# Optimization experiments

Measured on AMD Instinct MI355X. Metric: run time of the kernel, lower is better.

The kernel has to match this reference:

```python
import jax, jax.numpy as jnp
import numpy as np

B, IN_DIM, HID = 4096, 1024, 1024


def setup_inputs() -> dict:
    key = jax.random.key(0)
    ks = jax.random.split(key, 6)
    x_t = jax.random.normal(ks[0], (B, IN_DIM), dtype=jnp.float32)
    h_prev = jax.random.normal(ks[1], (B, HID), dtype=jnp.float32)
    c_prev = jax.random.normal(ks[2], (B, HID), dtype=jnp.float32)
    # stacked input-proj weights for gates (f, i, o, g): [4H, in_dim]
    U_w = jax.random.normal(ks[3], (4 * HID, IN_DIM), dtype=jnp.float32) * (1.0 / np.sqrt(IN_DIM))
    # biases: zeros except forget-gate bias = 1.0 (matches Uf.bias.fill_(1.0))
    U_b = jnp.concatenate([jnp.ones((HID,), jnp.float32), jnp.zeros((3 * HID,), jnp.float32)])
    # stacked hidden-proj weights (no bias): [4H, H]
    W_w = jax.random.normal(ks[4], (4 * HID, HID), dtype=jnp.float32) * (1.0 / np.sqrt(HID))
    return {"x_t": x_t, "h_prev": h_prev, "c_prev": c_prev,
            "U_w": U_w, "U_b": U_b, "W_w": W_w}


def reference(x_t, h_prev, c_prev, U_w, U_b, W_w):
    # two concatenated GEMMs covering all 8 original Linear layers
    pre = x_t @ U_w.T + U_b + h_prev @ W_w.T  # [B, 4H]
    f_pre, i_pre, o_pre, g_pre = jnp.split(pre, 4, axis=-1)
    f_t = jax.nn.sigmoid(f_pre)
    i_t = jax.nn.sigmoid(i_pre)
    o_t = jax.nn.sigmoid(o_pre)
    g_t = jnp.tanh(g_pre)
    c_t = f_t * c_prev + i_t * g_t
    h_t = o_t * jnp.tanh(c_t)
    return (h_t, c_t)
```

## Files before the change

### kernel.cpp

```cpp
#include <hip/hip_runtime.h>
#include <hip/hip_bf16.h>


#define BATCH 4096
#define HID   1024
#define KDIM  2048

#define BM 256
#define BN 256
#define BK 32
#define NT (KDIM / BK)
#define SLOT_E (BM * BK)

typedef __bf16 bf16x8 __attribute__((ext_vector_type(8)));
typedef float  f32x4  __attribute__((ext_vector_type(4)));

__device__ __forceinline__ void async_load16(const void* g, void* l) {
    __builtin_amdgcn_global_load_lds(
        (const __attribute__((address_space(1))) void*)g,
        (__attribute__((address_space(3))) void*)l,
        16, 0, 0);
}

__device__ __forceinline__ float sigmoidf_(float v) {
    return 1.0f / (1.0f + __expf(-v));
}
__device__ __forceinline__ float tanhf_(float v) {
    return 1.0f - 2.0f / (__expf(2.0f * v) + 1.0f);
}

__global__ __launch_bounds__(256) void convert_kernel(
    const float* __restrict__ x, const float* __restrict__ h,
    const float* __restrict__ U, const float* __restrict__ W,
    __hip_bfloat16* __restrict__ Acat, __hip_bfloat16* __restrict__ Bcat)
{
    const int CH_PER_MAT = (4096 * KDIM) / 8;
    int idx = blockIdx.x * blockDim.x + threadIdx.x;
    bool isB = idx >= CH_PER_MAT;
    int c = isB ? (idx - CH_PER_MAT) : idx;
    int row  = c >> 8;
    int col  = (c & 255) << 3;
    int srow = row;
    if (isB) {
        int g  = (row >> 4) & 3;
        int j  = ((row >> 8) << 6) + (((row >> 6) & 3) << 4) + (row & 15);
        srow = g * 1024 + j;
    }
    const float* src;
    if (col < 1024) src = (isB ? U : x) + (size_t)srow * 1024 + col;
    else            src = (isB ? W : h) + (size_t)srow * 1024 + (col - 1024);
    float4 v0 = *(const float4*)(src);
    float4 v1 = *(const float4*)(src + 4);
    __hip_bfloat16 tmp[8];
    tmp[0] = __float2bfloat16(v0.x); tmp[1] = __float2bfloat16(v0.y);
    tmp[2] = __float2bfloat16(v0.z); tmp[3] = __float2bfloat16(v0.w);
    tmp[4] = __float2bfloat16(v1.x); tmp[5] = __float2bfloat16(v1.y);
    tmp[6] = __float2bfloat16(v1.z); tmp[7] = __float2bfloat16(v1.w);
    __hip_bfloat16* dst = (isB ? Bcat : Acat) + (size_t)row * KDIM + col;
    *(bf16x8*)dst = *(const bf16x8*)tmp;
}

__global__ __launch_bounds__(512, 2) void gemm_lstm_kernel(
    const __hip_bfloat16* __restrict__ A,
    const __hip_bfloat16* __restrict__ Bm,
    const float* __restrict__ Ub,
    const float* __restrict__ c_prev,
    float* __restrict__ out)
{
    __shared__ __align__(16) __hip_bfloat16 smem[4 * 2 * SLOT_E];

    const int tid  = threadIdx.x;
    const int lane = tid & 63;
    const int wid  = tid >> 6;
    const int wm   = wid >> 2;
    const int wn   = wid & 3;

    int wg  = blockIdx.x;
    int wgs = (wg & 7) * (256 / 8) + (wg >> 3);
    const int bm = wgs >> 4;
    const int bn = wgs & 15;

    const __hip_bfloat16* Ab = A  + (size_t)bm * BM * KDIM;
    const __hip_bfloat16* Bb = Bm + (size_t)bn * BN * KDIM;

    const int frow = lane & 15;
    const int sp8  = (((lane >> 4) ^ ((frow >> 1) & 3)) << 3);
    const int arow = wm * 128 + frow;
    const int brow = wn * 64  + frow;

    const int c0 = tid,        c1 = 512 + tid;
    const int r0 = c0 >> 2,    r1 = c1 >> 2;
    const int g0 = ((c0 & 3) ^ ((r0 >> 1) & 3)) << 3;
    const int g1 = ((c1 & 3) ^ ((r1 >> 1) & 3)) << 3;
    const size_t ga0 = (size_t)r0 * KDIM + g0;
    const size_t ga1 = (size_t)r1 * KDIM + g1;
    const int l0 = c0 << 3,    l1 = c1 << 3;

    f32x4 acc[8][4] = {};

#define STAGE_A(kt, slot) do { \
    int _ko = (kt) * BK; unsigned _b = (unsigned)((slot) * 2 + 0) * SLOT_E; \
    async_load16(Ab + ga0 + _ko, &smem[_b + l0]); \
    async_load16(Ab + ga1 + _ko, &smem[_b + l1]); } while (0)
#define STAGE_B(kt, slot) do { \
    int _ko = (kt) * BK; unsigned _b = (unsigned)((slot) * 2 + 1) * SLOT_E; \
    async_load16(Bb + ga0 + _ko, &smem[_b + l0]); \
    async_load16(Bb + ga1 + _ko, &smem[_b + l1]); } while (0)

    STAGE_A(0, 0); STAGE_B(0, 0);
    STAGE_A(1, 1); STAGE_B(1, 1);
    STAGE_A(2, 2); STAGE_B(2, 2);
    asm volatile("s_waitcnt vmcnt(8)" ::: "memory");
    __builtin_amdgcn_s_barrier();

    for (int t = 0; t < NT; ++t) {
        const int slot = t & 3;
        const unsigned ab = (unsigned)(slot * 2 + 0) * SLOT_E;
        const unsigned bb = (unsigned)(slot * 2 + 1) * SLOT_E;
        int tp = t + 3; if (tp > NT - 1) tp = NT - 1;
        const int ps = (t + 3) & 3;

        STAGE_A(tp, ps);
        STAGE_B(tp, ps);

        bf16x8 ar[4], br[4];
#pragma unroll
        for (int m = 0; m < 4; ++m)
            ar[m] = *(const bf16x8*)&smem[ab + (unsigned)((arow + m * 16) * BK) + sp8];
#pragma unroll
        for (int n = 0; n < 4; ++n)
            br[n] = *(const bf16x8*)&smem[bb + (unsigned)((brow + n * 16) * BK) + sp8];

        __builtin_amdgcn_s_setprio(1);
#pragma unroll
        for (int m = 0; m < 4; ++m)
#pragma unroll
            for (int n = 0; n < 4; ++n)
                acc[m][n] = __builtin_amdgcn_mfma_f32_16x16x32_bf16(ar[m], br[n], acc[m][n], 0, 0, 0);
        __builtin_amdgcn_s_setprio(0);

        bf16x8 ar2[4];
#pragma unroll
        for (int m = 0; m < 4; ++m)
            ar2[m] = *(const bf16x8*)&smem[ab + (unsigned)((arow + 64 + m * 16) * BK) + sp8];

        __builtin_amdgcn_s_setprio(1);
#pragma unroll
        for (int m = 0; m < 4; ++m)
#pragma unroll
            for (int n = 0; n < 4; ++n)
                acc[m + 4][n] = __builtin_amdgcn_mfma_f32_16x16x32_bf16(ar2[m], br[n], acc[m + 4][n], 0, 0, 0);
        __builtin_amdgcn_s_setprio(0);

        asm volatile("s_waitcnt vmcnt(8)" ::: "memory");
        __builtin_amdgcn_s_barrier();
    }
#undef STAGE_A
#undef STAGE_B

    const int j = bn * 64 + wn * 16 + (lane & 15);
    const float bf_ = Ub[j];
    const float bi_ = Ub[1024 + j];
    const float bo_ = Ub[2048 + j];
    const float bg_ = Ub[3072 + j];
    const int row0 = bm * BM + wm * 128 + ((lane >> 4) << 2);

    float cp[8][4];
#pragma unroll
    for (int m = 0; m < 8; ++m)
#pragma unroll
        for (int r = 0; r < 4; ++r)
            cp[m][r] = c_prev[(size_t)(row0 + m * 16 + r) * HID + j];

#pragma unroll
    for (int m = 0; m < 8; ++m) {
#pragma unroll
        for (int r = 0; r < 4; ++r) {
            const int row = row0 + m * 16 + r;
            const float f  = sigmoidf_(acc[m][0][r] + bf_);
            const float it = sigmoidf_(acc[m][1][r] + bi_);
            const float o  = sigmoidf_(acc[m][2][r] + bo_);
            const float gg = tanhf_(acc[m][3][r] + bg_);
            const float cv = f * cp[m][r] + it * gg;
            const float hv = o * tanhf_(cv);
            out[(size_t)row * HID + j] = hv;
            out[(size_t)BATCH * HID + (size_t)row * HID + j] = cv;
        }
    }
}

extern "C" void kernel_launch(void* const* d_in, const int* in_sizes, int n_in,
                              void* d_out, int out_size, void* d_ws, size_t ws_size,
                              hipStream_t stream) {
    const float* x      = (const float*)d_in[0];
    const float* h_prev = (const float*)d_in[1];
    const float* c_prev = (const float*)d_in[2];
    const float* U_w    = (const float*)d_in[3];
    const float* U_b    = (const float*)d_in[4];
    const float* W_w    = (const float*)d_in[5];
    float* out = (float*)d_out;

    char* ws = (char*)d_ws;
    __hip_bfloat16* Acat = (__hip_bfloat16*)ws;
    __hip_bfloat16* Bcat = (__hip_bfloat16*)(ws + (16u << 20));

    convert_kernel<<<8192, 256, 0, stream>>>(x, h_prev, U_w, W_w, Acat, Bcat);
    gemm_lstm_kernel<<<256, 512, 0, stream>>>(Acat, Bcat, U_b, c_prev, out);
}
```

Baseline: 91.53 us.

## Restructure GEMM main loop into BK=64 ping-pong schedule with interleaved staging

Doubles the K tile to 64 and replaces the 4-slot ring buffer with two 64KB buffers. Each buffer holds A and B halves that are refilled per half-tile, interleaved between MFMA phases with explicit lgkm/vm waits and sched barriers. The even/odd register sets double-buffer the LDS fragment reads. The XCD-aware block mapping changes to group tiles into 4x8 regions, and launch bounds drop to one block per CU because of the 128KB LDS. The aim is better overlap of global loads, LDS reads and MFMAs and better L2 locality, at the cost of occupancy.

Result: faster. 83.62 us (-8.6%).

```diff
diff --git a/kernel.cpp b/kernel.cpp
--- a/kernel.cpp
+++ b/kernel.cpp
@@ -8,9 +8,8 @@
 
 #define BM 256
 #define BN 256
-#define BK 32
-#define NT (KDIM / BK)
-#define SLOT_E (BM * BK)
+#define BK 64
+#define NITER (KDIM / (2 * BK))
 
 typedef __bf16 bf16x8 __attribute__((ext_vector_type(8)));
 typedef float  f32x4  __attribute__((ext_vector_type(4)));
@@ -60,14 +59,14 @@
     *(bf16x8*)dst = *(const bf16x8*)tmp;
 }
 
-__global__ __launch_bounds__(512, 2) void gemm_lstm_kernel(
+__global__ __launch_bounds__(512, 1) void gemm_lstm_kernel(
     const __hip_bfloat16* __restrict__ A,
     const __hip_bfloat16* __restrict__ Bm,
     const float* __restrict__ Ub,
     const float* __restrict__ c_prev,
     float* __restrict__ out)
 {
-    __shared__ __align__(16) __hip_bfloat16 smem[4 * 2 * SLOT_E];
+    __shared__ __align__(16) unsigned char smem[131072];
 
     const int tid  = threadIdx.x;
     const int lane = tid & 63;
@@ -76,87 +75,124 @@
     const int wn   = wid & 3;
 
     int wg  = blockIdx.x;
-    int wgs = (wg & 7) * (256 / 8) + (wg >> 3);
-    const int bm = wgs >> 4;
-    const int bn = wgs & 15;
+    const int xcd = wg & 7;
+    const int i_  = wg >> 3;
+    const int bm = ((xcd >> 1) << 2) + (i_ >> 3);
+    const int bn = ((xcd & 1) << 3) + (i_ & 7);
 
     const __hip_bfloat16* Ab = A  + (size_t)bm * BM * KDIM;
     const __hip_bfloat16* Bb = Bm + (size_t)bn * BN * KDIM;
 
     const int frow = lane & 15;
-    const int sp8  = (((lane >> 4) ^ ((frow >> 1) & 3)) << 3);
-    const int arow = wm * 128 + frow;
-    const int brow = wn * 64  + frow;
-
-    const int c0 = tid,        c1 = 512 + tid;
-    const int r0 = c0 >> 2,    r1 = c1 >> 2;
-    const int g0 = ((c0 & 3) ^ ((r0 >> 1) & 3)) << 3;
-    const int g1 = ((c1 & 3) ^ ((r1 >> 1) & 3)) << 3;
-    const size_t ga0 = (size_t)r0 * KDIM + g0;
-    const size_t ga1 = (size_t)r1 * KDIM + g1;
-    const int l0 = c0 << 3,    l1 = c1 << 3;
+    const int kq   = lane >> 4;
+    const int esw  = (frow >> 1) & 7;
+    const unsigned xs0 = (unsigned)((kq ^ esw) << 4);
+    const unsigned xs1 = xs0 ^ 64u;
+    const unsigned wmBase = (unsigned)wm * 16384u;
+    const unsigned bnBase = (unsigned)(wn >> 1) * 16384u;
+    const unsigned bnRow  = (unsigned)(wn & 1) * 64u;
+
+    const int ch0 = tid,           ch1 = 512 + tid;
+    const int sr0 = ch0 >> 3,      sr1 = ch1 >> 3;
+    const int sc0 = ((ch0 & 7) ^ ((sr0 >> 1) & 7)) << 3;
+    const int sc1 = ((ch1 & 7) ^ ((sr1 >> 1) & 7)) << 3;
+    const size_t ga0 = (size_t)sr0 * KDIM + sc0;
+    const size_t ga1 = (size_t)sr1 * KDIM + sc1;
 
     f32x4 acc[8][4] = {};
-
-#define STAGE_A(kt, slot) do { \
-    int _ko = (kt) * BK; unsigned _b = (unsigned)((slot) * 2 + 0) * SLOT_E; \
-    async_load16(Ab + ga0 + _ko, &smem[_b + l0]); \
-    async_load16(Ab + ga1 + _ko, &smem[_b + l1]); } while (0)
-#define STAGE_B(kt, slot) do { \
-    int _ko = (kt) * BK; unsigned _b = (unsigned)((slot) * 2 + 1) * SLOT_E; \
-    async_load16(Bb + ga0 + _ko, &smem[_b + l0]); \
-    async_load16(Bb + ga1 + _ko, &smem[_b + l1]); } while (0)
-
-    STAGE_A(0, 0); STAGE_B(0, 0);
-    STAGE_A(1, 1); STAGE_B(1, 1);
-    STAGE_A(2, 2); STAGE_B(2, 2);
-    asm volatile("s_waitcnt vmcnt(8)" ::: "memory");
-    __builtin_amdgcn_s_barrier();
-
-    for (int t = 0; t < NT; ++t) {
-        const int slot = t & 3;
-        const unsigned ab = (unsigned)(slot * 2 + 0) * SLOT_E;
-        const unsigned bb = (unsigned)(slot * 2 + 1) * SLOT_E;
-        int tp = t + 3; if (tp > NT - 1) tp = NT - 1;
-        const int ps = (t + 3) & 3;
-
-        STAGE_A(tp, ps);
-        STAGE_B(tp, ps);
-
-        bf16x8 ar[4], br[4];
-#pragma unroll
-        for (int m = 0; m < 4; ++m)
-            ar[m] = *(const bf16x8*)&smem[ab + (unsigned)((arow + m * 16) * BK) + sp8];
-#pragma unroll
-        for (int n = 0; n < 4; ++n)
-            br[n] = *(const bf16x8*)&smem[bb + (unsigned)((brow + n * 16) * BK) + sp8];
-
-        __builtin_amdgcn_s_setprio(1);
-#pragma unroll
-        for (int m = 0; m < 4; ++m)
-#pragma unroll
-            for (int n = 0; n < 4; ++n)
-                acc[m][n] = __builtin_amdgcn_mfma_f32_16x16x32_bf16(ar[m], br[n], acc[m][n], 0, 0, 0);
-        __builtin_amdgcn_s_setprio(0);
-
-        bf16x8 ar2[4];
-#pragma unroll
-        for (int m = 0; m < 4; ++m)
-            ar2[m] = *(const bf16x8*)&smem[ab + (unsigned)((arow + 64 + m * 16) * BK) + sp8];
-
-        __builtin_amdgcn_s_setprio(1);
-#pragma unroll
-        for (int m = 0; m < 4; ++m)
-#pragma unroll
-            for (int n = 0; n < 4; ++n)
-                acc[m + 4][n] = __builtin_amdgcn_mfma_f32_16x16x32_bf16(ar2[m], br[n], acc[m + 4][n], 0, 0, 0);
-        __builtin_amdgcn_s_setprio(0);
-
-        asm volatile("s_waitcnt vmcnt(8)" ::: "memory");
-        __builtin_amdgcn_s_barrier();
+    bf16x8 arE[4], arO[4], brE[4], brO[4];
+
+#define RD16(B) (*(const bf16x8*)(smem + (B)))
+#define LDA4(SET, BUFB, MH, XS) do { \
+    const unsigned _b = (BUFB) + wmBase; \
+    SET[0] = RD16(_b + (unsigned)((MH)*64 +  0 + frow)*128u + (XS)); \
+    SET[1] = RD16(_b + (unsigned)((MH)*64 + 16 + frow)*128u + (XS)); \
+    SET[2] = RD16(_b + (unsigned)((MH)*64 + 32 + frow)*128u + (XS)); \
+    SET[3] = RD16(_b + (unsigned)((MH)*64 + 48 + frow)*128u + (XS)); } while (0)
+#define LDB4(SET, BUFB, XS) do { \
+    const unsigned _b = (BUFB) + 32768u + bnBase; \
+    SET[0] = RD16(_b + (bnRow +  0 + frow)*128u + (XS)); \
+    SET[1] = RD16(_b + (bnRow + 16 + frow)*128u + (XS)); \
+    SET[2] = RD16(_b + (bnRow + 32 + frow)*128u + (XS)); \
+    SET[3] = RD16(_b + (bnRow + 48 + frow)*128u + (XS)); } while (0)
+#define STG_A(TSRC, BUFB, H) do { \
+    const unsigned _rg = (BUFB) + (H)*16384u; \
+    const __hip_bfloat16* _s = Ab + (size_t)(H)*128*KDIM + (size_t)(TSRC)*64; \
+    async_load16(_s + ga0, smem + _rg + (unsigned)ch0*16u); \
+    async_load16(_s + ga1, smem + _rg + (unsigned)ch1*16u); } while (0)
+#define STG_B(TSRC, BUFB, H) do { \
+    const unsigned _rg = (BUFB) + 32768u + (H)*16384u; \
+    const __hip_bfloat16* _s = Bb + (size_t)(H)*128*KDIM + (size_t)(TSRC)*64; \
+    async_load16(_s + ga0, smem + _rg + (unsigned)ch0*16u); \
+    async_load16(_s + ga1, smem + _rg + (unsigned)ch1*16u); } while (0)
+#define MF16(ASET, BSET, MB) do { \
+    __builtin_amdgcn_s_setprio(1); \
+    _Pragma("unroll") for (int _m = 0; _m < 4; ++_m) \
+    _Pragma("unroll") for (int _n = 0; _n < 4; ++_n) \
+        acc[(MB)+_m][_n] = __builtin_amdgcn_mfma_f32_16x16x32_bf16( \
+            ASET[_m], BSET[_n], acc[(MB)+_m][_n], 0, 0, 0); \
+    __builtin_amdgcn_s_setprio(0); } while (0)
+#define DRAIN_LGKM asm volatile("s_waitcnt lgkmcnt(0)" ::: "memory")
+#define WAIT_VM4   asm volatile("s_waitcnt vmcnt(4)" ::: "memory")
+#define PH_BAR do { __builtin_amdgcn_sched_barrier(0); \
+                    __builtin_amdgcn_s_barrier(); } while (0)
+
+    STG_B(0, 0u, 0); STG_B(0, 0u, 1);
+    STG_A(0, 0u, 0); STG_A(0, 0u, 1);
+    STG_B(1, 65536u, 0); STG_B(1, 65536u, 1);
+    STG_A(1, 65536u, 0);
+    asm volatile("s_waitcnt vmcnt(6)" ::: "memory");
+    PH_BAR;
+    LDA4(arE, 0u, 0, xs0); LDB4(brE, 0u, xs0);
+
+#pragma unroll 1
+    for (int i = 0; i < NITER; ++i) {
+        const int tb = 2 * i + 1;
+        const int tc = (2 * i + 2 < 32) ? 2 * i + 2 : 31;
+        const int td = (2 * i + 3 < 32) ? 2 * i + 3 : 31;
+
+        LDA4(arO, 0u, 0, xs1); LDB4(brO, 0u, xs1);
+        STG_A(tb, 65536u, 1);
+        MF16(arE, brE, 0);
+        DRAIN_LGKM; PH_BAR;
+        LDA4(arE, 0u, 1, xs0);
+        STG_B(tc, 0u, 0);
+        MF16(arO, brO, 0);
+        PH_BAR;
+        LDA4(arO, 0u, 1, xs1);
+        STG_B(tc, 0u, 1);
+        MF16(arE, brE, 4);
+        DRAIN_LGKM; WAIT_VM4; PH_BAR;
+        LDA4(arE, 65536u, 0, xs0); LDB4(brE, 65536u, xs0);
+        STG_A(tc, 0u, 0);
+        MF16(arO, brO, 4);
+        PH_BAR;
+        LDA4(arO, 65536u, 0, xs1); LDB4(brO, 65536u, xs1);
+        STG_A(tc, 0u, 1);
+        MF16(arE, brE, 0);
+        DRAIN_LGKM; PH_BAR;
+        LDA4(arE, 65536u, 1, xs0);
+        STG_B(td, 65536u, 0);
+        MF16(arO, brO, 0);
+        PH_BAR;
+        LDA4(arO, 65536u, 1, xs1);
+        STG_B(td, 65536u, 1);
+        MF16(arE, brE, 4);
+        DRAIN_LGKM; WAIT_VM4; PH_BAR;
+        LDA4(arE, 0u, 0, xs0); LDB4(brE, 0u, xs0);
+        STG_A(td, 65536u, 0);
+        MF16(arO, brO, 4);
+        PH_BAR;
     }
-#undef STAGE_A
-#undef STAGE_B
+#undef RD16
+#undef LDA4
+#undef LDB4
+#undef STG_A
+#undef STG_B
+#undef MF16
+#undef DRAIN_LGKM
+#undef WAIT_VM4
+#undef PH_BAR
 
     const int j = bn * 64 + wn * 16 + (lane & 15);
     const float bf_ = Ub[j];
```

## Halve GEMM M-tile to 128, use triple-buffered LDS and XCD-aware tile mapping

Applied to the files above, without the earlier changes.

Cuts the GEMM block tile from 256x256 to 128x256 and doubles the grid to 512 workgroups. LDS drops to a 3-slot ring, launch bounds rise to 4 blocks per CU, and per-wave accumulators shrink from 8x4 to 4x4 fragments. The block-to-tile mapping is redone so each XCD covers a contiguous 8x8 region, with a new LDS swizzle. The aim is more parallelism and occupancy across CUs and better L2 locality. The cost is lower arithmetic intensity per tile, a shallower prefetch depth, and the removed setprio hints.

Result: slower. 94.67 us (+3.4%).

```diff
diff --git a/kernel.cpp b/kernel.cpp
--- a/kernel.cpp
+++ b/kernel.cpp
@@ -6,11 +6,11 @@
 #define HID   1024
 #define KDIM  2048
 
-#define BM 256
+#define BM 128
 #define BN 256
 #define BK 32
 #define NT (KDIM / BK)
-#define SLOT_E (BM * BK)
+#define SLOT_BYTES 24576u
 
 typedef __bf16 bf16x8 __attribute__((ext_vector_type(8)));
 typedef float  f32x4  __attribute__((ext_vector_type(4)));
@@ -60,14 +60,14 @@
     *(bf16x8*)dst = *(const bf16x8*)tmp;
 }
 
-__global__ __launch_bounds__(512, 2) void gemm_lstm_kernel(
+__global__ __launch_bounds__(512, 4) void gemm_lstm_kernel(
     const __hip_bfloat16* __restrict__ A,
     const __hip_bfloat16* __restrict__ Bm,
     const float* __restrict__ Ub,
     const float* __restrict__ c_prev,
     float* __restrict__ out)
 {
-    __shared__ __align__(16) __hip_bfloat16 smem[4 * 2 * SLOT_E];
+    __shared__ __align__(16) unsigned char smem[3 * SLOT_BYTES];
 
     const int tid  = threadIdx.x;
     const int lane = tid & 63;
@@ -76,104 +76,89 @@
     const int wn   = wid & 3;
 
     int wg  = blockIdx.x;
-    int wgs = (wg & 7) * (256 / 8) + (wg >> 3);
-    const int bm = wgs >> 4;
-    const int bn = wgs & 15;
+    const int xcd = wg & 7;
+    const int i_  = wg >> 3;
+    const int bm = ((xcd >> 1) << 3) + (i_ >> 3);
+    const int bn = ((xcd & 1) << 3) + (i_ & 7);
 
     const __hip_bfloat16* Ab = A  + (size_t)bm * BM * KDIM;
     const __hip_bfloat16* Bb = Bm + (size_t)bn * BN * KDIM;
 
     const int frow = lane & 15;
-    const int sp8  = (((lane >> 4) ^ ((frow >> 1) & 3)) << 3);
-    const int arow = wm * 128 + frow;
-    const int brow = wn * 64  + frow;
+    const int kq   = lane >> 4;
+    const int xw   = (frow ^ (frow >> 2)) & 3;
+    const unsigned sp = (unsigned)((kq ^ xw) << 4);
+    const unsigned arow = (unsigned)(wm * 64 + frow);
+    const unsigned brow = (unsigned)(wn * 64 + frow);
 
-    const int c0 = tid,        c1 = 512 + tid;
-    const int r0 = c0 >> 2,    r1 = c1 >> 2;
-    const int g0 = ((c0 & 3) ^ ((r0 >> 1) & 3)) << 3;
-    const int g1 = ((c1 & 3) ^ ((r1 >> 1) & 3)) << 3;
-    const size_t ga0 = (size_t)r0 * KDIM + g0;
-    const size_t ga1 = (size_t)r1 * KDIM + g1;
-    const int l0 = c0 << 3,    l1 = c1 << 3;
+    const int rA  = tid >> 2;
+    const int gA8 = (((tid & 3) ^ ((rA ^ (rA >> 2)) & 3)) << 3);
+    const size_t ga = (size_t)rA * KDIM + gA8;
 
-    f32x4 acc[8][4] = {};
+    f32x4 acc[4][4] = {};
 
-#define STAGE_A(kt, slot) do { \
-    int _ko = (kt) * BK; unsigned _b = (unsigned)((slot) * 2 + 0) * SLOT_E; \
-    async_load16(Ab + ga0 + _ko, &smem[_b + l0]); \
-    async_load16(Ab + ga1 + _ko, &smem[_b + l1]); } while (0)
-#define STAGE_B(kt, slot) do { \
-    int _ko = (kt) * BK; unsigned _b = (unsigned)((slot) * 2 + 1) * SLOT_E; \
-    async_load16(Bb + ga0 + _ko, &smem[_b + l0]); \
-    async_load16(Bb + ga1 + _ko, &smem[_b + l1]); } while (0)
+#define RD16(B) (*(const bf16x8*)(smem + (B)))
+#define STAGE(TSRC, SLOT) do { \
+    unsigned char* _b = smem + (SLOT) * SLOT_BYTES; \
+    const size_t _k = (size_t)(TSRC) * BK; \
+    async_load16(Ab + ga + _k, _b + (unsigned)tid * 16u); \
+    async_load16(Bb + ga + _k, _b + 8192u + (unsigned)tid * 16u); \
+    async_load16(Bb + ga + (size_t)128 * KDIM + _k, \
+                 _b + 16384u + (unsigned)tid * 16u); } while (0)
 
-    STAGE_A(0, 0); STAGE_B(0, 0);
-    STAGE_A(1, 1); STAGE_B(1, 1);
-    STAGE_A(2, 2); STAGE_B(2, 2);
-    asm volatile("s_waitcnt vmcnt(8)" ::: "memory");
+    STAGE(0, 0);
+    STAGE(1, 1);
+    asm volatile("s_waitcnt vmcnt(3)" ::: "memory");
     __builtin_amdgcn_s_barrier();
 
+    int s_cur = 0, s_dst = 2;
+#pragma unroll 1
     for (int t = 0; t < NT; ++t) {
-        const int slot = t & 3;
-        const unsigned ab = (unsigned)(slot * 2 + 0) * SLOT_E;
-        const unsigned bb = (unsigned)(slot * 2 + 1) * SLOT_E;
-        int tp = t + 3; if (tp > NT - 1) tp = NT - 1;
-        const int ps = (t + 3) & 3;
+        const int tsrc = (t + 2 < NT) ? (t + 2) : (NT - 1);
+        STAGE(tsrc, s_dst);
 
-        STAGE_A(tp, ps);
-        STAGE_B(tp, ps);
-
-        bf16x8 ar[4], br[4];
+        const unsigned ab = (unsigned)s_cur * SLOT_BYTES;
+        const unsigned bb = ab + 8192u;
+        bf16x8 af[4], bf[4];
 #pragma unroll
         for (int m = 0; m < 4; ++m)
-            ar[m] = *(const bf16x8*)&smem[ab + (unsigned)((arow + m * 16) * BK) + sp8];
+            af[m] = RD16(ab + (arow + m * 16u) * 64u + sp);
 #pragma unroll
         for (int n = 0; n < 4; ++n)
-            br[n] = *(const bf16x8*)&smem[bb + (unsigned)((brow + n * 16) * BK) + sp8];
+            bf[n] = RD16(bb + (brow + n * 16u) * 64u + sp);
 
-        __builtin_amdgcn_s_setprio(1);
 #pragma unroll
         for (int m = 0; m < 4; ++m)
 #pragma unroll
             for (int n = 0; n < 4; ++n)
-                acc[m][n] = __builtin_amdgcn_mfma_f32_16x16x32_bf16(ar[m], br[n], acc[m][n], 0, 0, 0);
-        __builtin_amdgcn_s_setprio(0);
+                acc[m][n] = __builtin_amdgcn_mfma_f32_16x16x32_bf16(
+                    af[m], bf[n], acc[m][n], 0, 0, 0);
 
-        bf16x8 ar2[4];
-#pragma unroll
-        for (int m = 0; m < 4; ++m)
-            ar2[m] = *(const bf16x8*)&smem[ab + (unsigned)((arow + 64 + m * 16) * BK) + sp8];
+        asm volatile("s_waitcnt vmcnt(3)" ::: "memory");
+        __builtin_amdgcn_s_barrier();
 
-        __builtin_amdgcn_s_setprio(1);
-#pragma unroll
-        for (int m = 0; m < 4; ++m)
-#pragma unroll
-            for (int n = 0; n < 4; ++n)
-                acc[m + 4][n] = __builtin_amdgcn_mfma_f32_16x16x32_bf16(ar2[m], br[n], acc[m + 4][n], 0, 0, 0);
-        __builtin_amdgcn_s_setprio(0);
+        s_cur = (s_cur == 2) ? 0 : s_cur + 1;
+        s_dst = (s_dst == 2) ? 0 : s_dst + 1;
+    }
+#undef RD16
+#undef STAGE
 
-        asm volatile("s_waitcnt vmcnt(8)" ::: "memory");
-        __builtin_amdgcn_s_barrier();
-    }
-#undef STAGE_A
-#undef STAGE_B
-
-    const int j = bn * 64 + wn * 16 + (lane & 15);
+    const int j = bn * 64 + wn * 16 + frow;
     const float bf_ = Ub[j];
     const float bi_ = Ub[1024 + j];
     const float bo_ = Ub[2048 + j];
     const float bg_ = Ub[3072 + j];
-    const int row0 = bm * BM + wm * 128 + ((lane >> 4) << 2);
+    const int row0 = bm * BM + wm * 64 + ((lane >> 4) << 2);
 
-    float cp[8][4];
+    float cp[4][4];
 #pragma unroll
-    for (int m = 0; m < 8; ++m)
+    for (int m = 0; m < 4; ++m)
 #pragma unroll
         for (int r = 0; r < 4; ++r)
             cp[m][r] = c_prev[(size_t)(row0 + m * 16 + r) * HID + j];
 
 #pragma unroll
-    for (int m = 0; m < 8; ++m) {
+    for (int m = 0; m < 4; ++m) {
 #pragma unroll
         for (int r = 0; r < 4; ++r) {
             const int row = row0 + m * 16 + r;
@@ -205,5 +190,5 @@
     __hip_bfloat16* Bcat = (__hip_bfloat16*)(ws + (16u << 20));
 
     convert_kernel<<<8192, 256, 0, stream>>>(x, h_prev, U_w, W_w, Acat, Bcat);
-    gemm_lstm_kernel<<<256, 512, 0, stream>>>(Acat, Bcat, U_b, c_prev, out);
+    gemm_lstm_kernel<<<512, 512, 0, stream>>>(Acat, Bcat, U_b, c_prev, out);
 }
```
